# Kernel tuning notes

Hardware: AMD Instinct MI355X
Metric: run time of the kernel (lower is better)

Reference implementation:

```python
import jax, jax.numpy as jnp
import numpy as np

N, D = 16384, 256

def setup_inputs() -> dict:
    key = jax.random.key(0)
    k1, k2, k3 = jax.random.split(key, 3)
    X = jax.random.normal(k1, (N, D), dtype=jnp.float32)
    W = jax.random.normal(k2, (D, D), dtype=jnp.float32) * (1.0 / np.sqrt(D))
    b = jax.random.normal(k3, (D,), dtype=jnp.float32) * (1.0 / np.sqrt(D))
    return {"X": X, "W": W, "b": b}

def reference(X, W, b):
    # Step 1: bilinear attention A = X W X^T   (N, N) -- materialized as in original
    A = (X @ W) @ X.T
    # Step 2: context aggregation Z = A X      (N, D)
    Z = A @ X
    # Step 3: output head g = Z b              (N,)
    g = Z @ b
    return g
```

## Files before the change

kernel.cpp:

```cpp
#include <hip/hip_runtime.h>

#define NROWS 16384
#define DDIM  256
#define K1BLK 2048
#define NSLOT 64


__global__ __launch_bounds__(256) void k1_v(const float* __restrict__ X,
                                            const float* __restrict__ b,
                                            float* __restrict__ slots) {
    const int tid  = threadIdx.x;
    const int lane = tid & 63;
    const int wave = tid >> 6;
    const int bid  = blockIdx.x;

    const float4* X4 = (const float4*)X;
    const float4  bf = ((const float4*)b)[lane];

    float4 vacc = make_float4(0.f, 0.f, 0.f, 0.f);
    const int row0 = bid * 8 + wave * 2;
    #pragma unroll
    for (int i = 0; i < 2; ++i) {
        const float4 xv = X4[(row0 + i) * 64 + lane];
        float t = xv.x * bf.x + xv.y * bf.y + xv.z * bf.z + xv.w * bf.w;
        #pragma unroll
        for (int off = 32; off; off >>= 1) t += __shfl_xor(t, off, 64);
        vacc.x += t * xv.x; vacc.y += t * xv.y;
        vacc.z += t * xv.z; vacc.w += t * xv.w;
    }

    __shared__ float sp[4][DDIM];
    ((float4*)sp[wave])[lane] = vacc;
    __syncthreads();
    const float s = sp[0][tid] + sp[1][tid] + sp[2][tid] + sp[3][tid];
    atomicAdd(&slots[(bid & (NSLOT - 1)) * DDIM + tid], s);
}

__global__ __launch_bounds__(256) void k2_w2(const float* __restrict__ slots,
                                             const float* __restrict__ W,
                                             float* __restrict__ w2) {
    const int tid  = threadIdx.x;
    const int lane = tid & 63;
    const int wave = tid >> 6;

    const float4* S4 = (const float4*)slots;
    float4 acc = make_float4(0.f, 0.f, 0.f, 0.f);
    const int r0 = wave * (NSLOT / 4);
    #pragma unroll
    for (int j = 0; j < NSLOT / 4; ++j) {
        const float4 p = S4[(r0 + j) * 64 + lane];
        acc.x += p.x; acc.y += p.y; acc.z += p.z; acc.w += p.w;
    }

    __shared__ float4 sp4[4][64];
    sp4[wave][lane] = acc;
    __syncthreads();

    const float* spf = (const float*)sp4;
    __shared__ __align__(16) float sv[DDIM];
    sv[tid] = spf[tid] + spf[256 + tid] + spf[512 + tid] + spf[768 + tid];
    __syncthreads();

    const float4 vf = ((const float4*)sv)[lane];
    const int row = blockIdx.x * 4 + wave;
    const float4 w = ((const float4*)W)[row * 64 + lane];
    float t = w.x * vf.x + w.y * vf.y + w.z * vf.z + w.w * vf.w;
    #pragma unroll
    for (int off = 32; off; off >>= 1) t += __shfl_xor(t, off, 64);
    if (lane == 0) w2[row] = t;
}

__global__ __launch_bounds__(256) void k3_g(const float* __restrict__ X,
                                            const float* __restrict__ w2,
                                            float* __restrict__ g) {
    const int tid  = threadIdx.x;
    const int lane = tid & 63;
    const int wave = tid >> 6;

    const float4* X4 = (const float4*)X;
    const float4  wf = ((const float4*)w2)[lane];

    const int row0 = blockIdx.x * 8 + wave * 2;
    #pragma unroll
    for (int i = 0; i < 2; ++i) {
        const float4 xv = X4[(row0 + i) * 64 + lane];
        float t = xv.x * wf.x + xv.y * wf.y + xv.z * wf.z + xv.w * wf.w;
        #pragma unroll
        for (int off = 32; off; off >>= 1) t += __shfl_xor(t, off, 64);
        if (lane == 0) g[row0 + i] = t;
    }
}

extern "C" void kernel_launch(void* const* d_in, const int* in_sizes, int n_in,
                              void* d_out, int out_size, void* d_ws, size_t ws_size,
                              hipStream_t stream) {
    const float* X = (const float*)d_in[0];
    const float* W = (const float*)d_in[1];
    const float* b = (const float*)d_in[2];
    float* out = (float*)d_out;

    float* slots = (float*)d_ws;
    float* w2    = slots + NSLOT * DDIM;

    k1_v <<<K1BLK, 256, 0, stream>>>(X, b, slots);
    k2_w2<<<NSLOT, 256, 0, stream>>>(slots, W, w2);
    k3_g <<<K1BLK, 256, 0, stream>>>(X, w2, out);
}
```

Measured before the change: 70.34 us.

## Fuse w2 computation into final g kernel, transposing W during first pass

Merges the small w2 = W·v kernel and the g = X·w2 kernel into one launch. Each of the 512 blocks redundantly reduces the 64 slots and computes the full w2 vector from a transposed copy of W, which the first kernel writes so the reads are coalesced. Every block then handles 32 rows of X instead of 8. This removes one kernel launch and one dependency boundary, but every block repeats the slot reduction and a 256x256 matrix-vector product, which adds redundant reads of Wt (mostly L2 hits). The first kernel also takes on a strided transposing write.

After: 79.77 us. 1.13x slower.

```diff
diff --git a/kernel.cpp b/kernel.cpp
--- a/kernel.cpp
+++ b/kernel.cpp
@@ -4,15 +4,20 @@
 #define DDIM  256
 #define K1BLK 2048
 #define NSLOT 64
+#define D2BLK 512
 
 
 __global__ __launch_bounds__(256) void k1_v(const float* __restrict__ X,
                                             const float* __restrict__ b,
-                                            float* __restrict__ slots) {
+                                            const float* __restrict__ W,
+                                            float* __restrict__ slots,
+                                            float* __restrict__ Wt) {
     const int tid  = threadIdx.x;
     const int lane = tid & 63;
     const int wave = tid >> 6;
     const int bid  = blockIdx.x;
+
+    if (bid < DDIM) Wt[tid * DDIM + bid] = W[bid * DDIM + tid];
 
     const float4* X4 = (const float4*)X;
     const float4  bf = ((const float4*)b)[lane];
@@ -36,12 +41,14 @@
     atomicAdd(&slots[(bid & (NSLOT - 1)) * DDIM + tid], s);
 }
 
-__global__ __launch_bounds__(256) void k2_w2(const float* __restrict__ slots,
-                                             const float* __restrict__ W,
-                                             float* __restrict__ w2) {
+__global__ __launch_bounds__(256) void k2_g(const float* __restrict__ slots,
+                                            const float* __restrict__ Wt,
+                                            const float* __restrict__ X,
+                                            float* __restrict__ g) {
     const int tid  = threadIdx.x;
     const int lane = tid & 63;
     const int wave = tid >> 6;
+    const int bid  = blockIdx.x;
 
     const float4* S4 = (const float4*)slots;
     float4 acc = make_float4(0.f, 0.f, 0.f, 0.f);
@@ -51,38 +58,31 @@
         const float4 p = S4[(r0 + j) * 64 + lane];
         acc.x += p.x; acc.y += p.y; acc.z += p.z; acc.w += p.w;
     }
-
     __shared__ float4 sp4[4][64];
     sp4[wave][lane] = acc;
     __syncthreads();
-
     const float* spf = (const float*)sp4;
     __shared__ __align__(16) float sv[DDIM];
     sv[tid] = spf[tid] + spf[256 + tid] + spf[512 + tid] + spf[768 + tid];
     __syncthreads();
 
-    const float4 vf = ((const float4*)sv)[lane];
-    const int row = blockIdx.x * 4 + wave;
-    const float4 w = ((const float4*)W)[row * 64 + lane];
-    float t = w.x * vf.x + w.y * vf.y + w.z * vf.z + w.w * vf.w;
+    float w2acc0 = 0.f, w2acc1 = 0.f, w2acc2 = 0.f, w2acc3 = 0.f;
+    #pragma unroll 4
+    for (int k = 0; k < DDIM; k += 4) {
+        w2acc0 += sv[k    ] * Wt[(k    ) * DDIM + tid];
+        w2acc1 += sv[k + 1] * Wt[(k + 1) * DDIM + tid];
+        w2acc2 += sv[k + 2] * Wt[(k + 2) * DDIM + tid];
+        w2acc3 += sv[k + 3] * Wt[(k + 3) * DDIM + tid];
+    }
+    __shared__ __align__(16) float sw2[DDIM];
+    sw2[tid] = (w2acc0 + w2acc1) + (w2acc2 + w2acc3);
+    __syncthreads();
+
+    const float4 wf = ((const float4*)sw2)[lane];
+    const float4* X4 = (const float4*)X;
+    const int row0 = bid * 32 + wave * 8;
     #pragma unroll
-    for (int off = 32; off; off >>= 1) t += __shfl_xor(t, off, 64);
-    if (lane == 0) w2[row] = t;
-}
-
-__global__ __launch_bounds__(256) void k3_g(const float* __restrict__ X,
-                                            const float* __restrict__ w2,
-                                            float* __restrict__ g) {
-    const int tid  = threadIdx.x;
-    const int lane = tid & 63;
-    const int wave = tid >> 6;
-
-    const float4* X4 = (const float4*)X;
-    const float4  wf = ((const float4*)w2)[lane];
-
-    const int row0 = blockIdx.x * 8 + wave * 2;
-    #pragma unroll
-    for (int i = 0; i < 2; ++i) {
+    for (int i = 0; i < 8; ++i) {
         const float4 xv = X4[(row0 + i) * 64 + lane];
         float t = xv.x * wf.x + xv.y * wf.y + xv.z * wf.z + xv.w * wf.w;
         #pragma unroll
@@ -100,9 +100,8 @@
     float* out = (float*)d_out;
 
     float* slots = (float*)d_ws;
-    float* w2    = slots + NSLOT * DDIM;
+    float* Wt    = slots + NSLOT * DDIM;
 
-    k1_v <<<K1BLK, 256, 0, stream>>>(X, b, slots);
-    k2_w2<<<NSLOT, 256, 0, stream>>>(slots, W, w2);
-    k3_g <<<K1BLK, 256, 0, stream>>>(X, w2, out);
+    k1_v<<<K1BLK, 256, 0, stream>>>(X, b, W, slots, Wt);
+    k2_g<<<D2BLK, 256, 0, stream>>>(slots, Wt, X, out);
 }
```
